# Kernel optimization log

Measured on AMD Instinct MI355X. Metric: run time of the kernel, lower is better.

Reference implementation:

```python
import jax, jax.numpy as jnp
import numpy as np

N, E = 50000, 500000
IN_C, HID, OUT_C, HEADS, NL = 128, 16, 16, 8, 4
EPS = 1e-5
NEG_SLOPE = 0.2


def _gatv2(x, src, dst, Wl, Wr, att, bias, concat):
    # GATv2Conv (PyG semantics, eval mode): lin_l on source, lin_r on target,
    # e = a . LeakyReLU(xl[src] + xr[dst]); segment softmax over dst; scatter-sum.
    n = x.shape[0]
    H, C = att.shape
    xl = (x @ Wl).reshape(n, H, C)
    xr = (x @ Wr).reshape(n, H, C)
    e = jax.nn.leaky_relu(xl[src] + xr[dst], NEG_SLOPE)          # [E', H, C]
    logit = jnp.einsum('ehc,hc->eh', e, att)                      # [E', H]
    mx = jax.lax.stop_gradient(jax.ops.segment_max(logit, dst, num_segments=n))
    a = jnp.exp(logit - mx[dst])
    denom = jax.ops.segment_sum(a, dst, num_segments=n)
    alpha = a / denom[dst]                                        # [E', H]
    out = jax.ops.segment_sum(xl[src] * alpha[..., None], dst, num_segments=n)
    out = out.reshape(n, H * C) if concat else out.mean(axis=1)
    return out + bias


def _bn_eval(x, g, b, m, v):
    return (x - m) * jax.lax.rsqrt(v + EPS) * g + b


def setup_inputs() -> dict:
    key = jax.random.key(0)
    ks = jax.random.split(key, 32)
    d = {}
    d['x'] = jax.random.normal(ks[0], (N, IN_C), dtype=jnp.float32)
    d['edge_index'] = jax.random.randint(ks[1], (2, E), 0, N, dtype=jnp.int64)
    HC = HID * HEADS  # 128
    dims_in = [IN_C, HC, HC, HC]
    dims_h = [HEADS, HEADS, HEADS, 1]
    dims_c = [HID, HID, HID, OUT_C]
    ki = 2
    for i in range(NL):
        fan = dims_in[i]
        s = 1.0 / np.sqrt(fan)
        d[f'W{i}l'] = jax.random.uniform(ks[ki], (fan, dims_h[i] * dims_c[i]), minval=-s, maxval=s, dtype=jnp.float32); ki += 1
        d[f'W{i}r'] = jax.random.uniform(ks[ki], (fan, dims_h[i] * dims_c[i]), minval=-s, maxval=s, dtype=jnp.float32); ki += 1
        d[f'a{i}'] = jax.random.normal(ks[ki], (dims_h[i], dims_c[i]), dtype=jnp.float32) * 0.1; ki += 1
        out_dim = dims_h[i] * dims_c[i] if i < NL - 1 else dims_c[i]
        d[f'b{i}'] = jnp.zeros((out_dim,), dtype=jnp.float32)
    for i in range(NL - 1):
        d[f'g{i}'] = jnp.ones((HC,), dtype=jnp.float32) + 0.1 * jax.random.normal(ks[ki], (HC,), dtype=jnp.float32); ki += 1
        d[f'be{i}'] = 0.1 * jax.random.normal(ks[ki], (HC,), dtype=jnp.float32); ki += 1
        d[f'm{i}'] = 0.1 * jax.random.normal(ks[ki], (HC,), dtype=jnp.float32); ki += 1
        d[f'v{i}'] = jnp.ones((HC,), dtype=jnp.float32)
    return d


def reference(x, edge_index, W0l, W0r, a0, b0, W1l, W1r, a1, b1, W2l, W2r, a2, b2, W3l, W3r, a3, b3, g0, be0, m0, v0, g1, be1, m1, v1, g2, be2, m2, v2):
    n = x.shape[0]
    loop = jnp.arange(n, dtype=edge_index.dtype)
    src = jnp.concatenate([edge_index[0], loop])  # add_self_loops=True (PyG default)
    dst = jnp.concatenate([edge_index[1], loop])
    Ws = [(W0l, W0r, a0, b0), (W1l, W1r, a1, b1), (W2l, W2r, a2, b2), (W3l, W3r, a3, b3)]
    bns = [(g0, be0, m0, v0), (g1, be1, m1, v1), (g2, be2, m2, v2)]
    h = x
    for i in range(NL):
        Wl, Wr, att, bias = Ws[i]
        h = _gatv2(h, src, dst, Wl, Wr, att, bias, concat=(i < NL - 1))
        if i < NL - 1:
            g, b, m, v = bns[i]
            h = jax.nn.elu(_bn_eval(h, g, b, m, v))
    return h
```

## Files before the change

kernel.cpp:

```cpp
#include <hip/hip_runtime.h>
#include <hip/hip_fp16.h>
#include <math.h>

static constexpr float BN_EPS = 1e-5f;
static constexpr float NEG = 0.2f;

typedef float f32x4 __attribute__((ext_vector_type(4)));
typedef _Float16 h16x2 __attribute__((ext_vector_type(2)));
typedef _Float16 h16x8 __attribute__((ext_vector_type(8)));


__global__ __launch_bounds__(256) void hist_pack(
    const int* __restrict__ ei, int E, int n, int* __restrict__ cnt,
    const float* __restrict__ W0l, const float* __restrict__ W0r,
    const float* __restrict__ W1l, const float* __restrict__ W1r,
    const float* __restrict__ W2l, const float* __restrict__ W2r,
    const float* __restrict__ W3l, const float* __restrict__ W3r,
    __half* __restrict__ pk0, __half* __restrict__ pk1,
    __half* __restrict__ pk2, __half* __restrict__ pk3) {
    int b = blockIdx.x;
    if (b < 200) {
        if (threadIdx.x >= 64) return;
        const float *Wl, *Wr;
        __half* packed;
        int tile, NTT, M;
        if (b < 192) {
            int layer = b >> 6;
            tile = b & 63;
            NTT = 16; M = 128;
            Wl = (layer == 0) ? W0l : (layer == 1) ? W1l : W2l;
            Wr = (layer == 0) ? W0r : (layer == 1) ? W1r : W2r;
            packed = (layer == 0) ? pk0 : (layer == 1) ? pk1 : pk2;
        } else {
            tile = b - 192;
            NTT = 2; M = 16;
            Wl = W3l; Wr = W3r; packed = pk3;
        }
        int NT = NTT >> 1;
        int gnt = tile % NTT;
        int kt = tile / NTT;
        int l = threadIdx.x;
        const float* W = (gnt < NT) ? Wl : Wr;
        int col = (gnt % NT) * 16 + (l & 15);
        int krow = kt * 32 + ((l >> 4) << 3);
        size_t base = (size_t)tile * 512 + (size_t)l * 8;
#pragma unroll
        for (int j = 0; j < 8; j++)
            packed[base + j] = __float2half(W[(size_t)(krow + j) * M + col]);
    } else {
        int e = (b - 200) * 256 + threadIdx.x;
        int ET = E + n;
        if (e >= ET) return;
        int d = (e < E) ? ei[E + e] : (e - E);
        atomicAdd(&cnt[d], 1);
    }
}


__device__ __forceinline__ void scan_block_body256(
    const int* __restrict__ cnt, int* __restrict__ rowptr,
    int* __restrict__ bsums, int n, int bid, int* s) {
    int t = threadIdx.x;
    int base = bid * 1024 + t * 4;
    int v0 = 0, v1 = 0, v2 = 0, v3 = 0;
    if (base + 3 < n) {
        v0 = cnt[base];     v1 = cnt[base + 1];
        v2 = cnt[base + 2]; v3 = cnt[base + 3];
    } else {
        if (base < n)     v0 = cnt[base];
        if (base + 1 < n) v1 = cnt[base + 1];
        if (base + 2 < n) v2 = cnt[base + 2];
        if (base + 3 < n) v3 = cnt[base + 3];
    }
    int p1 = v0 + v1, p2 = p1 + v2, p3 = p2 + v3;
    s[t] = p3;
    __syncthreads();
    for (int d = 1; d < 256; d <<= 1) {
        int tt = (t >= d) ? s[t - d] : 0;
        __syncthreads();
        s[t] += tt;
        __syncthreads();
    }
    int ex = s[t] - p3;
    if (base < n)     rowptr[base + 1] = ex + v0;
    if (base + 1 < n) rowptr[base + 2] = ex + p1;
    if (base + 2 < n) rowptr[base + 3] = ex + p2;
    if (base + 3 < n) rowptr[base + 4] = ex + p3;
    if (t == 255) bsums[bid] = s[255];
}

__global__ __launch_bounds__(1024) void scan_add2(
    int* __restrict__ rowptr, const int* __restrict__ bsums, int n, int nb) {
    __shared__ int sex;
    if (threadIdx.x < 64) {
        int L = threadIdx.x;
        int v = (L < nb) ? bsums[L] : 0;
#pragma unroll
        for (int d = 1; d < 64; d <<= 1) {
            int t = __shfl_up(v, d);
            if (L >= d) v += t;
        }
        int ex = __shfl_up(v, 1);
        if (L == 0) ex = 0;
        if (L == (int)blockIdx.x) sex = ex;
    }
    __syncthreads();
    int i = blockIdx.x * 1024 + threadIdx.x;
    if (i < n) rowptr[i + 1] += sex;
    if (i == 0) rowptr[0] = 0;
}

__global__ void scatter_kernel(const int* __restrict__ ei, int E, int n,
                               const int* __restrict__ rowptr, int* __restrict__ fill,
                               int* __restrict__ col) {
    int e = blockIdx.x * blockDim.x + threadIdx.x;
    int ET = E + n;
    if (e >= ET) return;
    int s, d;
    if (e < E) { s = ei[e]; d = ei[E + e]; } else { s = e - E; d = s; }
    int pos = atomicAdd(&fill[d], 1);
    col[rowptr[d] + pos] = s;
}


template <bool FIRST>
__device__ __forceinline__ void gemm_body(
    const __half* __restrict__ xh, const float* __restrict__ xf,
    const __half* __restrict__ packed,
    __half* __restrict__ Y1, __half* __restrict__ Y2, int n, int bid,
    _Float16* sA) {
    const int t = threadIdx.x;
    const int row0 = bid * 64;

    for (int c = t; c < 1024; c += 256) {
        int row = c >> 4;
        int off = (c & 15) * 8;
        int gr = row0 + row;
        if (gr >= n) gr = n - 1;
        if (FIRST) {
            float4 v0 = *(const float4*)&xf[(size_t)gr * 128 + off];
            float4 v1 = *(const float4*)&xf[(size_t)gr * 128 + off + 4];
            h16x8 h = {(_Float16)v0.x, (_Float16)v0.y, (_Float16)v0.z, (_Float16)v0.w,
                       (_Float16)v1.x, (_Float16)v1.y, (_Float16)v1.z, (_Float16)v1.w};
            *(h16x8*)&sA[row * 136 + off] = h;
        } else {
            *(h16x8*)&sA[row * 136 + off] = *(const h16x8*)&xh[(size_t)gr * 128 + off];
        }
    }
    __syncthreads();

    const int lane = t & 63;
    const int s = t >> 6;
    const int lr = lane & 15;
    const int kq = (lane >> 4) * 8;

    h16x8 af[4][4];
#pragma unroll
    for (int rt = 0; rt < 4; rt++)
#pragma unroll
        for (int kt = 0; kt < 4; kt++)
            af[rt][kt] = *(const h16x8*)&sA[(rt * 16 + lr) * 136 + kt * 32 + kq];

    f32x4 acc[4][4];
#pragma unroll
    for (int a = 0; a < 4; a++)
#pragma unroll
        for (int b = 0; b < 4; b++) acc[a][b] = (f32x4){0.f, 0.f, 0.f, 0.f};

#pragma unroll
    for (int kt = 0; kt < 4; kt++) {
#pragma unroll
        for (int ntl = 0; ntl < 4; ntl++) {
            int nt = s * 4 + ntl;
            h16x8 b = *(const h16x8*)&packed[((size_t)(kt * 16 + nt)) * 512 + lane * 8];
#pragma unroll
            for (int rt = 0; rt < 4; rt++)
                acc[ntl][rt] = __builtin_amdgcn_mfma_f32_16x16x32_f16(af[rt][kt], b, acc[ntl][rt], 0, 0, 0);
        }
    }

    __half* Y = (s < 2) ? Y1 : Y2;
    const int colh = (s & 1) * 64;
    const int rq = (lane >> 4) * 4;
#pragma unroll
    for (int ntl = 0; ntl < 4; ntl++) {
        int col = colh + ntl * 16 + lr;
#pragma unroll
        for (int rt = 0; rt < 4; rt++) {
#pragma unroll
            for (int g = 0; g < 4; g++) {
                int row = row0 + rt * 16 + rq + g;
                if (row < n) Y[(size_t)row * 128 + col] = __float2half(acc[ntl][rt][g]);
            }
        }
    }
}

__global__ __launch_bounds__(256) void gemm_h_big2(
    const __half* __restrict__ xh, const __half* __restrict__ packed,
    __half* __restrict__ Y1, __half* __restrict__ Y2, int n) {
    __shared__ __align__(16) char smem[64 * 136 * 2];
    gemm_body<false>(xh, nullptr, packed, Y1, Y2, n, blockIdx.x, (_Float16*)smem);
}

__global__ __launch_bounds__(256) void scanblk_gemm0(
    const int* __restrict__ cnt, int* __restrict__ rowptr,
    int* __restrict__ bsums, int n, int nscan,
    const float* __restrict__ xf, const __half* __restrict__ packed,
    __half* __restrict__ Y1, __half* __restrict__ Y2) {
    __shared__ __align__(16) char smem[64 * 136 * 2];
    int b = blockIdx.x;
    if (b < nscan) {
        scan_block_body256(cnt, rowptr, bsums, n, b, (int*)smem);
    } else {
        gemm_body<true>(nullptr, xf, packed, Y1, Y2, n, b - nscan,
                        (_Float16*)smem);
    }
}


__global__ __launch_bounds__(256) void gemm_h_small(
    const __half* __restrict__ xh, const __half* __restrict__ packed,
    float* __restrict__ Y1, float* __restrict__ Y2, int n) {
    int lane = threadIdx.x & 63;
    int wv = blockIdx.x * 4 + (threadIdx.x >> 6);
    int row0 = wv * 16;
    if (row0 >= n) return;
    int r = row0 + (lane & 15);
    if (r >= n) r = n - 1;
    int kq = (lane >> 4) * 8;

    h16x8 af[4];
#pragma unroll
    for (int kt = 0; kt < 4; kt++)
        af[kt] = *(const h16x8*)&xh[(size_t)r * 128 + kt * 32 + kq];

    f32x4 acc[2];
    acc[0] = (f32x4){0.f, 0.f, 0.f, 0.f};
    acc[1] = (f32x4){0.f, 0.f, 0.f, 0.f};

#pragma unroll
    for (int kt = 0; kt < 4; kt++) {
#pragma unroll
        for (int nt = 0; nt < 2; nt++) {
            h16x8 b = *(const h16x8*)&packed[((size_t)(kt * 2 + nt)) * 512 + lane * 8];
            acc[nt] = __builtin_amdgcn_mfma_f32_16x16x32_f16(af[kt], b, acc[nt], 0, 0, 0);
        }
    }

    int colb = lane & 15;
    int rbase = row0 + (lane >> 4) * 4;
#pragma unroll
    for (int nt = 0; nt < 2; nt++) {
        float* Y = (nt == 0) ? Y1 : Y2;
#pragma unroll
        for (int g = 0; g < 4; g++) {
            int row = rbase + g;
            if (row < n) Y[(size_t)row * 16 + colb] = acc[nt][g];
        }
    }
}


__device__ __forceinline__ float dot8_h(const h16x2* lp, const h16x2* ap) {
#if __has_builtin(__builtin_amdgcn_fdot2)
    float part = __builtin_amdgcn_fdot2(lp[0], ap[0], 0.f, false);
    part = __builtin_amdgcn_fdot2(lp[1], ap[1], part, false);
    part = __builtin_amdgcn_fdot2(lp[2], ap[2], part, false);
    return __builtin_amdgcn_fdot2(lp[3], ap[3], part, false);
#else
    float part = 0.f;
#pragma unroll
    for (int i = 0; i < 4; i++)
        part += (float)lp[i].x * (float)ap[i].x + (float)lp[i].y * (float)ap[i].y;
    return part;
#endif
}

__global__ __launch_bounds__(256) void agg_h(
    const __half* __restrict__ xl, const __half* __restrict__ xr,
    const int* __restrict__ rowptr, const int* __restrict__ col,
    const float* __restrict__ att, const float* __restrict__ bias,
    const float* __restrict__ g, const float* __restrict__ be,
    const float* __restrict__ bm, const float* __restrict__ bv,
    __half* __restrict__ oh, int n) {
    int v = (blockIdx.x * blockDim.x + threadIdx.x) >> 6;
    if (v >= n) return;
    int lane = threadIdx.x & 63;
    int grp = lane >> 4;
    int L = lane & 15;
    int ch = L * 8;

    int beg = rowptr[v];
    int end = rowptr[v + 1];
    int cb = beg;
    int cidx = (cb + lane < end) ? col[cb + lane] : v;

    h16x8 rx = *(const h16x8*)&xr[((size_t)v << 7) + ch];
    float4 av0 = *(const float4*)&att[ch];
    float4 av1 = *(const float4*)&att[ch + 4];
    h16x2 a[4] = {{(_Float16)av0.x, (_Float16)av0.y},
                  {(_Float16)av0.z, (_Float16)av0.w},
                  {(_Float16)av1.x, (_Float16)av1.y},
                  {(_Float16)av1.z, (_Float16)av1.w}};
    const h16x8 neg8 = {(_Float16)NEG, (_Float16)NEG, (_Float16)NEG, (_Float16)NEG,
                        (_Float16)NEG, (_Float16)NEG, (_Float16)NEG, (_Float16)NEG};

    float lrun = 0.f;
    float acc[8] = {0.f, 0.f, 0.f, 0.f, 0.f, 0.f, 0.f, 0.f};

    auto proc = [&](h16x8 hv, bool ok) {
        h16x8 s = hv + rx;
        h16x8 l = __builtin_elementwise_max(s, s * neg8);
        const h16x2* lp = (const h16x2*)&l;
        float part = dot8_h(lp, a);
        part += __shfl_xor(part, 1);
        float p = ok ? __expf(part) : 0.f;
        lrun += p;
        const _Float16* hp = (const _Float16*)&hv;
#pragma unroll
        for (int k = 0; k < 8; k++) acc[k] = fmaf(p, (float)hp[k], acc[k]);
    };

    while (true) {
        int ce = min(end, cb + 64);
        for (int e = cb; e < ce; e += 16) {
            int off = e - cb;
            h16x8 hv[4];
#pragma unroll
            for (int j = 0; j < 4; j++) {
                int u = __shfl(cidx, off + 4 * j + grp);
                hv[j] = *(const h16x8*)&xl[((size_t)u << 7) + ch];
            }
#pragma unroll
            for (int j = 0; j < 4; j++) proc(hv[j], e + 4 * j + grp < ce);
        }
        cb += 64;
        if (cb >= end) break;
        cidx = (cb + lane < end) ? col[cb + lane] : v;
    }

    lrun += __shfl_xor(lrun, 16);
    lrun += __shfl_xor(lrun, 32);
#pragma unroll
    for (int k = 0; k < 8; k++) {
        acc[k] += __shfl_xor(acc[k], 16);
        acc[k] += __shfl_xor(acc[k], 32);
    }

    float inv = 1.0f / lrun;
    int c2 = ch + 2 * grp;
    float2 b2 = *(const float2*)&bias[c2];
    float2 m2 = *(const float2*)&bm[c2];
    float2 v2 = *(const float2*)&bv[c2];
    float2 g2 = *(const float2*)&g[c2];
    float2 e2 = *(const float2*)&be[c2];
    float bbv[2] = {b2.x, b2.y}, msv[2] = {m2.x, m2.y}, vsv[2] = {v2.x, v2.y};
    float gsv[2] = {g2.x, g2.y}, esv[2] = {e2.x, e2.y};
    unsigned short hs[2];
#pragma unroll
    for (int j = 0; j < 2; j++) {
        float o = fmaf(acc[2 * grp + j], inv, bbv[j]);
        o = (o - msv[j]) * rsqrtf(vsv[j] + BN_EPS) * gsv[j] + esv[j];
        o = o > 0.f ? o : expm1f(o);
        hs[j] = __half_as_ushort(__float2half(o));
    }
    *(ushort2*)&oh[((size_t)v << 7) + c2] = make_ushort2(hs[0], hs[1]);
}


__global__ __launch_bounds__(256) void agg_f(
    const float* __restrict__ xl, const float* __restrict__ xr,
    const int* __restrict__ rowptr, const int* __restrict__ col,
    const float* __restrict__ att, const float* __restrict__ bias,
    float* __restrict__ out, int n) {
    int v = (blockIdx.x * blockDim.x + threadIdx.x) >> 6;
    if (v >= n) return;
    int lane = threadIdx.x & 63;
    int slot = lane >> 2;
    int L = lane & 3;
    int ch = 4 * L;

    int beg = rowptr[v];
    int end = rowptr[v + 1];
    int cb = beg;
    int cidx = (cb + lane < end) ? col[cb + lane] : v;

    float4 xrv = *(const float4*)&xr[((size_t)v << 4) + ch];
    float4 av = *(const float4*)&att[ch];

    float lrun = 0.f;
    float4 acc = make_float4(0.f, 0.f, 0.f, 0.f);

    while (true) {
        int ce = min(end, cb + 64);
        for (int e = cb; e < ce; e += 16) {
            bool ok = (e + slot < ce);
            int u = __shfl(cidx, e - cb + slot);
            float4 xv = *(const float4*)&xl[((size_t)u << 4) + ch];
            float s0 = xv.x + xrv.x; s0 = s0 > 0.f ? s0 : NEG * s0;
            float s1 = xv.y + xrv.y; s1 = s1 > 0.f ? s1 : NEG * s1;
            float s2 = xv.z + xrv.z; s2 = s2 > 0.f ? s2 : NEG * s2;
            float s3 = xv.w + xrv.w; s3 = s3 > 0.f ? s3 : NEG * s3;
            float part = fmaf(s0, av.x, fmaf(s1, av.y, fmaf(s2, av.z, s3 * av.w)));
            part += __shfl_xor(part, 1);
            part += __shfl_xor(part, 2);
            float p = ok ? __expf(part) : 0.f;
            lrun += p;
            acc.x = fmaf(p, xv.x, acc.x);
            acc.y = fmaf(p, xv.y, acc.y);
            acc.z = fmaf(p, xv.z, acc.z);
            acc.w = fmaf(p, xv.w, acc.w);
        }
        cb += 64;
        if (cb >= end) break;
        cidx = (cb + lane < end) ? col[cb + lane] : v;
    }

#pragma unroll
    for (int d = 4; d < 64; d <<= 1) {
        lrun += __shfl_xor(lrun, d);
        acc.x += __shfl_xor(acc.x, d);
        acc.y += __shfl_xor(acc.y, d);
        acc.z += __shfl_xor(acc.z, d);
        acc.w += __shfl_xor(acc.w, d);
    }

    if (slot == 0) {
        float inv = 1.0f / lrun;
        float4 b4 = *(const float4*)&bias[ch];
        *(float4*)&out[((size_t)v << 4) + ch] =
            make_float4(fmaf(acc.x, inv, b4.x), fmaf(acc.y, inv, b4.y),
                        fmaf(acc.z, inv, b4.z), fmaf(acc.w, inv, b4.w));
    }
}


extern "C" void kernel_launch(void* const* d_in, const int* in_sizes, int n_in,
                              void* d_out, int out_size, void* d_ws, size_t ws_size,
                              hipStream_t stream) {
    const float* x = (const float*)d_in[0];
    const int* ei = (const int*)d_in[1];
    const float* Wl[4] = {(const float*)d_in[2], (const float*)d_in[6],
                          (const float*)d_in[10], (const float*)d_in[14]};
    const float* Wr[4] = {(const float*)d_in[3], (const float*)d_in[7],
                          (const float*)d_in[11], (const float*)d_in[15]};
    const float* att[4] = {(const float*)d_in[4], (const float*)d_in[8],
                           (const float*)d_in[12], (const float*)d_in[16]};
    const float* bias[4] = {(const float*)d_in[5], (const float*)d_in[9],
                            (const float*)d_in[13], (const float*)d_in[17]};
    const float* g[3] = {(const float*)d_in[18], (const float*)d_in[22], (const float*)d_in[26]};
    const float* be[3] = {(const float*)d_in[19], (const float*)d_in[23], (const float*)d_in[27]};
    const float* bm[3] = {(const float*)d_in[20], (const float*)d_in[24], (const float*)d_in[28]};
    const float* bv[3] = {(const float*)d_in[21], (const float*)d_in[25], (const float*)d_in[29]};

    const int n = in_sizes[0] / 128;
    const int E = in_sizes[1] / 2;
    const int ET = E + n;

    char* p = (char*)d_ws;
    __half* xh = (__half*)p;           p += (size_t)n * 128 * 2;
    __half* xlh = (__half*)p;          p += (size_t)n * 128 * 2;
    __half* xrh = (__half*)p;          p += (size_t)n * 128 * 2;
    float* xl3 = (float*)p;            p += (size_t)n * 16 * 4;
    float* xr3 = (float*)p;            p += (size_t)n * 16 * 4;
    int* rowptr = (int*)p;            p += (size_t)(n + 4) * 4;
    int* cnt = (int*)p;               p += (size_t)n * 4;
    int* fill = (int*)p;              p += (size_t)n * 4;
    int* col = (int*)p;               p += (size_t)ET * 4;
    int* bsums = (int*)p;             p += 256;
    __half* pk[4];
    for (int i = 0; i < 3; i++) { pk[i] = (__half*)p; p += 4 * 16 * 512 * 2; }
    pk[3] = (__half*)p;               p += 4 * 2 * 512 * 2;

    (void)hipMemsetAsync(cnt, 0, (size_t)n * 8, stream);

    const int tb = 256;
    const int histBlocks = (ET + tb - 1) / tb;
    hist_pack<<<200 + histBlocks, tb, 0, stream>>>(
        ei, E, n, cnt,
        Wl[0], Wr[0], Wl[1], Wr[1], Wl[2], Wr[2], Wl[3], Wr[3],
        pk[0], pk[1], pk[2], pk[3]);

    const int nb = (n + 1023) / 1024;
    const int gb64 = (n + 63) / 64;
    const int gemmBlocksSmall = ((n + 15) / 16 + 3) / 4;
    const int aggBlocks = (n + 3) / 4;

    scanblk_gemm0<<<nb + gb64, 256, 0, stream>>>(
        cnt, rowptr, bsums, n, nb, x, pk[0], xlh, xrh);
    scan_add2<<<nb, 1024, 0, stream>>>(rowptr, bsums, n, nb);
    scatter_kernel<<<(ET + tb - 1) / tb, tb, 0, stream>>>(ei, E, n, rowptr, fill, col);

    agg_h<<<aggBlocks, 256, 0, stream>>>(
        xlh, xrh, rowptr, col, att[0], bias[0], g[0], be[0], bm[0], bv[0], xh, n);
    for (int i = 1; i < 3; i++) {
        gemm_h_big2<<<gb64, 256, 0, stream>>>(xh, pk[i], xlh, xrh, n);
        agg_h<<<aggBlocks, 256, 0, stream>>>(
            xlh, xrh, rowptr, col, att[i], bias[i], g[i], be[i], bm[i], bv[i], xh, n);
    }
    gemm_h_small<<<gemmBlocksSmall, 256, 0, stream>>>(xh, pk[3], xl3, xr3, n);
    agg_f<<<aggBlocks, 256, 0, stream>>>(
        xl3, xr3, rowptr, col, att[3], bias[3], (float*)d_out, n);
}
```

Before: 369.3 us.

## Map one node per 16-lane group in aggregation and precompute folded BN affine

The aggregation kernels now give each destination node a 16-lane group (agg_h) or a 4-lane group (agg_f) instead of a full 64-lane wavefront. This removes the cross-group shuffle reductions and stops lanes idling on low-degree nodes, since the average degree is about 11. Bias and eval-mode batchnorm are folded into per-channel A/B coefficients, computed once in an extra block of the hist/pack kernel, so the epilogue becomes a single fma. The trade-off is that each node's edges are walked serially four at a time with fewer loads in flight per node, and warps can diverge when degrees differ between the nodes sharing a wavefront.

Result: faster. 329.6 us (-10.7%).

```diff
diff --git a/kernel.cpp b/kernel.cpp
--- a/kernel.cpp
+++ b/kernel.cpp
@@ -17,7 +17,18 @@
     const float* __restrict__ W2l, const float* __restrict__ W2r,
     const float* __restrict__ W3l, const float* __restrict__ W3r,
     __half* __restrict__ pk0, __half* __restrict__ pk1,
-    __half* __restrict__ pk2, __half* __restrict__ pk3) {
+    __half* __restrict__ pk2, __half* __restrict__ pk3,
+    const float* __restrict__ b0, const float* __restrict__ b1,
+    const float* __restrict__ b2,
+    const float* __restrict__ g0, const float* __restrict__ g1,
+    const float* __restrict__ g2,
+    const float* __restrict__ be0, const float* __restrict__ be1,
+    const float* __restrict__ be2,
+    const float* __restrict__ m0, const float* __restrict__ m1,
+    const float* __restrict__ m2,
+    const float* __restrict__ v0, const float* __restrict__ v1,
+    const float* __restrict__ v2,
+    float* __restrict__ bnA, float* __restrict__ bnB) {
     int b = blockIdx.x;
     if (b < 200) {
         if (threadIdx.x >= 64) return;
@@ -47,8 +58,21 @@
 #pragma unroll
         for (int j = 0; j < 8; j++)
             packed[base + j] = __float2half(W[(size_t)(krow + j) * M + col]);
+    } else if (b == 200) {
+        for (int t = threadIdx.x; t < 384; t += 256) {
+            int layer = t >> 7;
+            int c = t & 127;
+            const float* gg = (layer == 0) ? g0 : (layer == 1) ? g1 : g2;
+            const float* ee = (layer == 0) ? be0 : (layer == 1) ? be1 : be2;
+            const float* mm = (layer == 0) ? m0 : (layer == 1) ? m1 : m2;
+            const float* vv = (layer == 0) ? v0 : (layer == 1) ? v1 : v2;
+            const float* bb = (layer == 0) ? b0 : (layer == 1) ? b1 : b2;
+            float A = gg[c] * rsqrtf(vv[c] + BN_EPS);
+            bnA[t] = A;
+            bnB[t] = fmaf(bb[c] - mm[c], A, ee[c]);
+        }
     } else {
-        int e = (b - 200) * 256 + threadIdx.x;
+        int e = (b - 201) * 256 + threadIdx.x;
         int ET = E + n;
         if (e >= ET) return;
         int d = (e < E) ? ei[E + e] : (e - E);
@@ -280,21 +304,18 @@
 __global__ __launch_bounds__(256) void agg_h(
     const __half* __restrict__ xl, const __half* __restrict__ xr,
     const int* __restrict__ rowptr, const int* __restrict__ col,
-    const float* __restrict__ att, const float* __restrict__ bias,
-    const float* __restrict__ g, const float* __restrict__ be,
-    const float* __restrict__ bm, const float* __restrict__ bv,
+    const float* __restrict__ att,
+    const float* __restrict__ bnA, const float* __restrict__ bnB,
     __half* __restrict__ oh, int n) {
-    int v = (blockIdx.x * blockDim.x + threadIdx.x) >> 6;
+    int v = (blockIdx.x * blockDim.x + threadIdx.x) >> 4;
     if (v >= n) return;
-    int lane = threadIdx.x & 63;
-    int grp = lane >> 4;
-    int L = lane & 15;
+    int L = threadIdx.x & 15;
     int ch = L * 8;
 
     int beg = rowptr[v];
     int end = rowptr[v + 1];
     int cb = beg;
-    int cidx = (cb + lane < end) ? col[cb + lane] : v;
+    int cidx = (cb + L < end) ? col[cb + L] : v;
 
     h16x8 rx = *(const h16x8*)&xr[((size_t)v << 7) + ch];
     float4 av0 = *(const float4*)&att[ch];
@@ -323,49 +344,38 @@
     };
 
     while (true) {
-        int ce = min(end, cb + 64);
-        for (int e = cb; e < ce; e += 16) {
+        int ce = min(end, cb + 16);
+        for (int e = cb; e < ce; e += 4) {
             int off = e - cb;
             h16x8 hv[4];
 #pragma unroll
             for (int j = 0; j < 4; j++) {
-                int u = __shfl(cidx, off + 4 * j + grp);
+                int u = __shfl(cidx, off + j, 16);
                 hv[j] = *(const h16x8*)&xl[((size_t)u << 7) + ch];
             }
 #pragma unroll
-            for (int j = 0; j < 4; j++) proc(hv[j], e + 4 * j + grp < ce);
-        }
-        cb += 64;
+            for (int j = 0; j < 4; j++) proc(hv[j], e + j < end);
+        }
+        cb += 16;
         if (cb >= end) break;
-        cidx = (cb + lane < end) ? col[cb + lane] : v;
-    }
-
-    lrun += __shfl_xor(lrun, 16);
-    lrun += __shfl_xor(lrun, 32);
+        cidx = (cb + L < end) ? col[cb + L] : v;
+    }
+
+    float inv = 1.0f / lrun;
+    float4 A0 = *(const float4*)&bnA[ch];
+    float4 A1 = *(const float4*)&bnA[ch + 4];
+    float4 B0 = *(const float4*)&bnB[ch];
+    float4 B1 = *(const float4*)&bnB[ch + 4];
+    float Av[8] = {A0.x, A0.y, A0.z, A0.w, A1.x, A1.y, A1.z, A1.w};
+    float Bv[8] = {B0.x, B0.y, B0.z, B0.w, B1.x, B1.y, B1.z, B1.w};
+    h16x8 outv;
 #pragma unroll
     for (int k = 0; k < 8; k++) {
-        acc[k] += __shfl_xor(acc[k], 16);
-        acc[k] += __shfl_xor(acc[k], 32);
-    }
-
-    float inv = 1.0f / lrun;
-    int c2 = ch + 2 * grp;
-    float2 b2 = *(const float2*)&bias[c2];
-    float2 m2 = *(const float2*)&bm[c2];
-    float2 v2 = *(const float2*)&bv[c2];
-    float2 g2 = *(const float2*)&g[c2];
-    float2 e2 = *(const float2*)&be[c2];
-    float bbv[2] = {b2.x, b2.y}, msv[2] = {m2.x, m2.y}, vsv[2] = {v2.x, v2.y};
-    float gsv[2] = {g2.x, g2.y}, esv[2] = {e2.x, e2.y};
-    unsigned short hs[2];
-#pragma unroll
-    for (int j = 0; j < 2; j++) {
-        float o = fmaf(acc[2 * grp + j], inv, bbv[j]);
-        o = (o - msv[j]) * rsqrtf(vsv[j] + BN_EPS) * gsv[j] + esv[j];
+        float o = fmaf(acc[k], inv * Av[k], Bv[k]);
         o = o > 0.f ? o : expm1f(o);
-        hs[j] = __half_as_ushort(__float2half(o));
-    }
-    *(ushort2*)&oh[((size_t)v << 7) + c2] = make_ushort2(hs[0], hs[1]);
+        outv[k] = (_Float16)o;
+    }
+    *(h16x8*)&oh[((size_t)v << 7) + ch] = outv;
 }
 
 
@@ -374,17 +384,15 @@
     const int* __restrict__ rowptr, const int* __restrict__ col,
     const float* __restrict__ att, const float* __restrict__ bias,
     float* __restrict__ out, int n) {
-    int v = (blockIdx.x * blockDim.x + threadIdx.x) >> 6;
+    int v = (blockIdx.x * blockDim.x + threadIdx.x) >> 2;
     if (v >= n) return;
-    int lane = threadIdx.x & 63;
-    int slot = lane >> 2;
-    int L = lane & 3;
+    int L = threadIdx.x & 3;
     int ch = 4 * L;
 
     int beg = rowptr[v];
     int end = rowptr[v + 1];
     int cb = beg;
-    int cidx = (cb + lane < end) ? col[cb + lane] : v;
+    int cidx = (cb + L < end) ? col[cb + L] : v;
 
     float4 xrv = *(const float4*)&xr[((size_t)v << 4) + ch];
     float4 av = *(const float4*)&att[ch];
@@ -393,46 +401,39 @@
     float4 acc = make_float4(0.f, 0.f, 0.f, 0.f);
 
     while (true) {
-        int ce = min(end, cb + 64);
-        for (int e = cb; e < ce; e += 16) {
-            bool ok = (e + slot < ce);
-            int u = __shfl(cidx, e - cb + slot);
-            float4 xv = *(const float4*)&xl[((size_t)u << 4) + ch];
-            float s0 = xv.x + xrv.x; s0 = s0 > 0.f ? s0 : NEG * s0;
-            float s1 = xv.y + xrv.y; s1 = s1 > 0.f ? s1 : NEG * s1;
-            float s2 = xv.z + xrv.z; s2 = s2 > 0.f ? s2 : NEG * s2;
-            float s3 = xv.w + xrv.w; s3 = s3 > 0.f ? s3 : NEG * s3;
+        float4 xv[4];
+#pragma unroll
+        for (int j = 0; j < 4; j++) {
+            int u = __shfl(cidx, j, 4);
+            xv[j] = *(const float4*)&xl[((size_t)u << 4) + ch];
+        }
+#pragma unroll
+        for (int j = 0; j < 4; j++) {
+            bool ok = (cb + j < end);
+            float s0 = xv[j].x + xrv.x; s0 = s0 > 0.f ? s0 : NEG * s0;
+            float s1 = xv[j].y + xrv.y; s1 = s1 > 0.f ? s1 : NEG * s1;
+            float s2 = xv[j].z + xrv.z; s2 = s2 > 0.f ? s2 : NEG * s2;
+            float s3 = xv[j].w + xrv.w; s3 = s3 > 0.f ? s3 : NEG * s3;
             float part = fmaf(s0, av.x, fmaf(s1, av.y, fmaf(s2, av.z, s3 * av.w)));
             part += __shfl_xor(part, 1);
             part += __shfl_xor(part, 2);
             float p = ok ? __expf(part) : 0.f;
             lrun += p;
-            acc.x = fmaf(p, xv.x, acc.x);
-            acc.y = fmaf(p, xv.y, acc.y);
-            acc.z = fmaf(p, xv.z, acc.z);
-            acc.w = fmaf(p, xv.w, acc.w);
-        }
-        cb += 64;
+            acc.x = fmaf(p, xv[j].x, acc.x);
+            acc.y = fmaf(p, xv[j].y, acc.y);
+            acc.z = fmaf(p, xv[j].z, acc.z);
+            acc.w = fmaf(p, xv[j].w, acc.w);
+        }
+        cb += 4;
         if (cb >= end) break;
-        cidx = (cb + lane < end) ? col[cb + lane] : v;
-    }
-
-#pragma unroll
-    for (int d = 4; d < 64; d <<= 1) {
-        lrun += __shfl_xor(lrun, d);
-        acc.x += __shfl_xor(acc.x, d);
-        acc.y += __shfl_xor(acc.y, d);
-        acc.z += __shfl_xor(acc.z, d);
-        acc.w += __shfl_xor(acc.w, d);
-    }
-
-    if (slot == 0) {
-        float inv = 1.0f / lrun;
-        float4 b4 = *(const float4*)&bias[ch];
-        *(float4*)&out[((size_t)v << 4) + ch] =
-            make_float4(fmaf(acc.x, inv, b4.x), fmaf(acc.y, inv, b4.y),
-                        fmaf(acc.z, inv, b4.z), fmaf(acc.w, inv, b4.w));
-    }
+        cidx = (cb + L < end) ? col[cb + L] : v;
+    }
+
+    float inv = 1.0f / lrun;
+    float4 b4 = *(const float4*)&bias[ch];
+    *(float4*)&out[((size_t)v << 4) + ch] =
+        make_float4(fmaf(acc.x, inv, b4.x), fmaf(acc.y, inv, b4.y),
+                    fmaf(acc.z, inv, b4.z), fmaf(acc.w, inv, b4.w));
 }
 
 
@@ -472,34 +473,41 @@
     __half* pk[4];
     for (int i = 0; i < 3; i++) { pk[i] = (__half*)p; p += 4 * 16 * 512 * 2; }
     pk[3] = (__half*)p;               p += 4 * 2 * 512 * 2;
+    float* bnA = (float*)p;           p += 384 * 4;
+    float* bnB = (float*)p;           p += 384 * 4;
 
     (void)hipMemsetAsync(cnt, 0, (size_t)n * 8, stream);
 
     const int tb = 256;
     const int histBlocks = (ET + tb - 1) / tb;
-    hist_pack<<<200 + histBlocks, tb, 0, stream>>>(
+    hist_pack<<<201 + histBlocks, tb, 0, stream>>>(
         ei, E, n, cnt,
         Wl[0], Wr[0], Wl[1], Wr[1], Wl[2], Wr[2], Wl[3], Wr[3],
-        pk[0], pk[1], pk[2], pk[3]);
+        pk[0], pk[1], pk[2], pk[3],
+        bias[0], bias[1], bias[2],
+        g[0], g[1], g[2], be[0], be[1], be[2],
+        bm[0], bm[1], bm[2], bv[0], bv[1], bv[2],
+        bnA, bnB);
 
     const int nb = (n + 1023) / 1024;
     const int gb64 = (n + 63) / 64;
     const int gemmBlocksSmall = ((n + 15) / 16 + 3) / 4;
-    const int aggBlocks = (n + 3) / 4;
+    const int aggBlocksH = (n + 15) / 16;
+    const int aggBlocksF = (n + 63) / 64;
 
     scanblk_gemm0<<<nb + gb64, 256, 0, stream>>>(
         cnt, rowptr, bsums, n, nb, x, pk[0], xlh, xrh);
     scan_add2<<<nb, 1024, 0, stream>>>(rowptr, bsums, n, nb);
     scatter_kernel<<<(ET + tb - 1) / tb, tb, 0, stream>>>(ei, E, n, rowptr, fill, col);
 
-    agg_h<<<aggBlocks, 256, 0, stream>>>(
-        xlh, xrh, rowptr, col, att[0], bias[0], g[0], be[0], bm[0], bv[0], xh, n);
+    agg_h<<<aggBlocksH, 256, 0, stream>>>(
+        xlh, xrh, rowptr, col, att[0], bnA, bnB, xh, n);
     for (int i = 1; i < 3; i++) {
         gemm_h_big2<<<gb64, 256, 0, stream>>>(xh, pk[i], xlh, xrh, n);
-        agg_h<<<aggBlocks, 256, 0, stream>>>(
-            xlh, xrh, rowptr, col, att[i], bias[i], g[i], be[i], bm[i], bv[i], xh, n);
+        agg_h<<<aggBlocksH, 256, 0, stream>>>(
+            xlh, xrh, rowptr, col, att[i], bnA + 128 * i, bnB + 128 * i, xh, n);
     }
     gemm_h_small<<<gemmBlocksSmall, 256, 0, stream>>>(xh, pk[3], xl3, xr3, n);
-    agg_f<<<aggBlocks, 256, 0, stream>>>(
+    agg_f<<<aggBlocksF, 256, 0, stream>>>(
         xl3, xr3, rowptr, col, att[3], bias[3], (float*)d_out, n);
 }
```
